# Kernel tuning notes

Measured on AMD Instinct MI355X. Metric: run time of the kernel, lower is better.

## Reference

```python
import jax, jax.numpy as jnp
import numpy as np

N, DZ, L, H, MLPH, INC = 256, 256, 256, 512, 2048, 8
CAT_IDX = np.arange(0, 192, 2)                      # 96 categorical token positions (interleaved)
NUM_IDX = np.setdiff1d(np.arange(L), CAT_IDX)       # 160 numerical token positions
CARDS = [4, 16, 128]                                # cardinality per categorical group
GSZ = 32                                            # tokens per categorical group
NUM_CARD = 100                                      # cardinality of quantized numerical params


def setup_inputs() -> dict:
    ks = list(jax.random.split(jax.random.key(0), 24))
    def nrm(shape, s=0.02):
        return jax.random.normal(ks.pop(), shape, jnp.float32) * s
    inp = {}
    inp['z'] = jax.random.normal(ks.pop(), (N, DZ), jnp.float32)
    inp['mlp_w0'] = nrm((DZ, MLPH)); inp['mlp_b0'] = jnp.zeros((MLPH,), jnp.float32)
    inp['mlp_w1'] = nrm((MLPH, MLPH)); inp['mlp_b1'] = jnp.zeros((MLPH,), jnp.float32)
    inp['mlp_w2'] = nrm((MLPH, MLPH)); inp['mlp_b2'] = jnp.zeros((MLPH,), jnp.float32)
    inp['conv_w'] = nrm((H, INC)); inp['conv_b'] = jnp.zeros((H,), jnp.float32)
    for g, card in enumerate(CARDS):
        inp[f'cat_w{g}'] = nrm((H, card)); inp[f'cat_b{g}'] = jnp.zeros((card,), jnp.float32)
    inp['num_w'] = nrm((H, 2)); inp['num_b'] = jnp.zeros((2,), jnp.float32)
    inp['num_target'] = jax.random.uniform(ks.pop(), (N, len(NUM_IDX)), jnp.float32)
    inp['cat_target'] = jax.random.randint(ks.pop(), (N, len(CAT_IDX)), 0, 4, jnp.int32)
    return inp


def reference(z, mlp_w0, mlp_b0, mlp_w1, mlp_b1, mlp_w2, mlp_b2, conv_w, conv_b,
              cat_w0, cat_b0, cat_w1, cat_b1, cat_w2, cat_b2, num_w, num_b,
              num_target, cat_target):
    n = z.shape[0]
    # MLP: fc0 -> act -> fc1 -> act -> fc2
    h = z @ mlp_w0 + mlp_b0
    h = jax.nn.relu(h) @ mlp_w1 + mlp_b1
    h = jax.nn.relu(h) @ mlp_w2 + mlp_b2
    h = h.reshape(n, INC, L)                        # (N, C=8, L)
    # act + 1x1 conv to hidden_size, then transpose -> (N, L, H)
    u = jnp.einsum('ncl,hc->nlh', jax.nn.relu(h), conv_w) + conv_b
    # ---- categorical tokens: gather, per-cardinality heads, CE NLL, argmax sample ----
    hc = u[:, CAT_IDX, :]                           # (N, 96, H)
    heads = [(cat_w0, cat_b0), (cat_w1, cat_b1), (cat_w2, cat_b2)]
    nlls, samps = [], []
    for g, (w, b) in enumerate(heads):
        hg = hc[:, g * GSZ:(g + 1) * GSZ, :]        # (N, 32, H)
        logits = hg @ w + b                         # (N, 32, card)
        logp = jax.nn.log_softmax(logits, axis=-1)
        tg = cat_target[:, g * GSZ:(g + 1) * GSZ]
        nlls.append(-jnp.take_along_axis(logp, tg[..., None], axis=-1)[..., 0])
        samps.append(jnp.argmax(logits, axis=-1))
    cat_nll = jnp.concatenate(nlls, axis=1)         # (N, 96)
    cat_samples = jnp.concatenate(samps, axis=1)    # (N, 96)
    # ---- numerical tokens: gather, 2-param discretized logistic, NLL, mode sample ----
    hn = u[:, NUM_IDX, :]                           # (N, 160, H)
    p = hn @ num_w + num_b                          # (N, 160, 2)
    mu = jax.nn.sigmoid(p[..., 0])
    s = jax.nn.softplus(p[..., 1]) + 1e-4
    hb = 1.0 / (2.0 * (NUM_CARD - 1))               # half bin width
    t = num_target
    cdf_p = jax.nn.sigmoid((t + hb - mu) / s)
    cdf_m = jax.nn.sigmoid((t - hb - mu) / s)
    prob = jnp.where(t < hb, cdf_p, jnp.where(t > 1.0 - hb, 1.0 - cdf_m, cdf_p - cdf_m))
    num_nll = -jnp.log(jnp.maximum(prob, 1e-7))     # (N, 160)
    num_samples = jax.lax.stop_gradient(jnp.round(mu * (NUM_CARD - 1)) / (NUM_CARD - 1))
    # ---- scatter samples back into the preallocated output tensor ----
    u_out = jnp.zeros((n, L, 3), jnp.float32)
    u_out = u_out.at[:, CAT_IDX, 0].set(cat_samples.astype(jnp.float32))
    u_out = u_out.at[:, NUM_IDX, 1].set(num_samples)
    return u_out, cat_nll, num_nll
```

## Files before the change

### kernel.cpp

```cpp
#include <hip/hip_runtime.h>
#include <hip/hip_fp16.h>
#include <math.h>

#define NN   256
#define LL   256
#define HH   512
#define MLPHv 2048
#define INCv 8
#define NCOLS 150

typedef _Float16 f16x8 __attribute__((ext_vector_type(8)));
typedef __fp16   fp16x2 __attribute__((ext_vector_type(2)));
typedef float    f32x4 __attribute__((ext_vector_type(4)));
typedef unsigned short ushort_t;

union u4f16 { uint4 u; f16x8 v; };
union u1f16 { fp16x2 h; unsigned u; };

__device__ __forceinline__ void split1(float f, ushort_t& h, ushort_t& l)
{
    __half hh = __float2half_rn(f);
    h = __half_as_ushort(hh);
    l = __half_as_ushort(__float2half_rn((f - __half2float(hh)) * 4096.f));
}

__device__ __forceinline__ void pack8(const float* fv, uint4& hv, uint4& lv)
{
    unsigned hw[4], lw[4];
#pragma unroll
    for (int p = 0; p < 4; ++p) {
        const float a = fv[2 * p], b = fv[2 * p + 1];
        u1f16 hc, lc;
        hc.h = __builtin_amdgcn_cvt_pkrtz(a, b);
        const float r0 = (a - (float)hc.h[0]) * 4096.f;
        const float r1 = (b - (float)hc.h[1]) * 4096.f;
        lc.h = __builtin_amdgcn_cvt_pkrtz(r0, r1);
        hw[p] = hc.u;
        lw[p] = lc.u;
    }
    hv.x = hw[0]; hv.y = hw[1]; hv.z = hw[2]; hv.w = hw[3];
    lv.x = lw[0]; lv.y = lw[1]; lv.z = lw[2]; lv.w = lw[3];
}

typedef __attribute__((address_space(3))) unsigned int lds_u32;
typedef __attribute__((address_space(1))) const unsigned int glb_u32;
__device__ __forceinline__ void gl_lds16(const ushort_t* g, ushort_t* l)
{
    __builtin_amdgcn_global_load_lds((glb_u32*)g, (lds_u32*)l, 16, 0, 0);
}
__device__ __forceinline__ void gl_lds16f(const float* g, float* l)
{
    __builtin_amdgcn_global_load_lds((glb_u32*)g, (lds_u32*)l, 16, 0, 0);
}


__global__ __launch_bounds__(256) void prep_small(
    const float* __restrict__ z,
    const float* __restrict__ cvw, const float* __restrict__ cvb,
    const float* __restrict__ cw0, const float* __restrict__ cb0,
    const float* __restrict__ cw1, const float* __restrict__ cb1,
    const float* __restrict__ cw2, const float* __restrict__ cb2,
    const float* __restrict__ nw,  const float* __restrict__ nbv,
    ushort_t* __restrict__ zh, ushort_t* __restrict__ zl,
    float* __restrict__ Mf, float* __restrict__ beta)
{
    const int bid = blockIdx.x;
    const int tid = threadIdx.x;
    if (bid < 16) {
        const int idx = bid * 256 + tid;
        const int r = idx >> 4, kq = idx & 15;
        const float* p = z + (size_t)r * 256 + kq * 16;
        float fv[16];
#pragma unroll
        for (int q = 0; q < 4; ++q) {
            float4 v = *(const float4*)(p + q * 4);
            fv[q * 4 + 0] = v.x; fv[q * 4 + 1] = v.y;
            fv[q * 4 + 2] = v.z; fv[q * 4 + 3] = v.w;
        }
        const int gm = r >> 4, l16 = r & 15;
#pragma unroll
        for (int o = 0; o < 2; ++o) {
            uint4 hv, lv;
            pack8(&fv[o * 8], hv, lv);
            const int koct = kq * 2 + o;
            const int ks = koct >> 2, koct3 = koct & 3;
            const size_t off = ((size_t)(gm * 8 + ks) * 64 + l16 + (koct3 << 4)) * 8;
            *(uint4*)&zh[off] = hv;
            *(uint4*)&zl[off] = lv;
        }
    } else {
        const int k = bid - 16;
        const float* W; const float* B; int off, card;
        if (k < 4)        { W = cw0; B = cb0; off = 0;   card = 4;   }
        else if (k < 20)  { W = cw1; B = cb1; off = 4;   card = 16;  }
        else if (k < 148) { W = cw2; B = cb2; off = 20;  card = 128; }
        else              { W = nw;  B = nbv; off = 148; card = 2;   }
        const int kc = k - off;
        float part[INCv + 1];
#pragma unroll
        for (int c = 0; c <= INCv; ++c) part[c] = 0.f;
#pragma unroll
        for (int it = 0; it < 2; ++it) {
            const int h = tid + it * 256;
            const float wv = W[h * card + kc];
#pragma unroll
            for (int c = 0; c < INCv; ++c) part[c] += cvw[h * INCv + c] * wv;
            part[INCv] += cvb[h] * wv;
        }
        __shared__ float red[INCv + 1][4];
        const int lane = tid & 63, wave = tid >> 6;
#pragma unroll
        for (int c = 0; c <= INCv; ++c) {
            float v = part[c];
#pragma unroll
            for (int o = 32; o >= 1; o >>= 1) v += __shfl_down(v, o, 64);
            if (lane == 0) red[c][wave] = v;
        }
        __syncthreads();
        if (tid <= INCv) {
            const float s = red[tid][0] + red[tid][1] + red[tid][2] + red[tid][3];
            if (tid < INCv) Mf[tid * NCOLS + k] = s;
            else            beta[k] = s + B[kc];
        }
    }
}

template <int OUT>
__global__ __launch_bounds__(512, 2) void gemm_v3(
    const ushort_t* __restrict__ Ah, const ushort_t* __restrict__ Al,
    const float* __restrict__ W, const float* __restrict__ bias,
    float* __restrict__ part, ushort_t* __restrict__ oH, ushort_t* __restrict__ oL,
    int KS32, int kchunk32, int steps)
{
    __shared__ ushort_t sAh[2][4096];
    __shared__ ushort_t sAl[2][4096];
    __shared__ float    sWf[2][4160];

    const int tid  = threadIdx.x;
    const int lane = tid & 63, w = tid >> 6;
    const int wr   = w >> 2, wc = w & 3;
    const int bx   = blockIdx.x, by = blockIdx.y, bz = blockIdx.z;
    const int bn   = bx * 64;
    const int kb0  = bz * kchunk32;

    f32x4 accH[2], accC[2];
#pragma unroll
    for (int r = 0; r < 2; ++r) {
        accH[r] = (f32x4){0.f, 0.f, 0.f, 0.f};
        accC[r] = (f32x4){0.f, 0.f, 0.f, 0.f};
    }

    auto STAGE = [&](int ts, int b) {
        const int kb = kb0 + ts * 2;
        const int g = w >> 1, ks = w & 1;
        const size_t fA = ((size_t)(by * 4 + g) * KS32 + kb + ks) * 512 + lane * 8;
        gl_lds16(Ah + fA, &sAh[b][w * 512]);
        gl_lds16(Al + fA, &sAl[b][w * 512]);
        const int k0 = kb * 32;
#pragma unroll
        for (int ii = 0; ii < 2; ++ii) {
            const int i = w * 2 + ii;
            const float* src = W + (size_t)(k0 + i * 4 + (lane >> 4)) * 2048 + bn + (lane & 15) * 4;
            gl_lds16f(src, &sWf[b][i * 260]);
        }
    };

    STAGE(0, 0);
    for (int t = 0; t < steps; ++t) {
        const int cur = t & 1;
        if (t + 1 < steps) {
            STAGE(t + 1, cur ^ 1);
            asm volatile("s_waitcnt vmcnt(4)" ::: "memory");
        } else {
            asm volatile("s_waitcnt vmcnt(0)" ::: "memory");
        }
        __builtin_amdgcn_s_barrier();
        asm volatile("" ::: "memory");

        f16x8 bH[2], bL[2];
#pragma unroll
        for (int ks = 0; ks < 2; ++ks) {
            const int col  = wc * 16 + (lane & 15);
            const int koct = lane >> 4;
            float fv[8];
#pragma unroll
            for (int j = 0; j < 8; ++j) {
                const int i = ks * 8 + koct * 2 + (j >> 2);
                fv[j] = sWf[cur][i * 260 + (j & 3) * 64 + col];
            }
            u4f16 hv, lv;
            pack8(fv, hv.u, lv.u);
            bH[ks] = hv.v;
            bL[ks] = lv.v;
        }

        __builtin_amdgcn_s_setprio(1);
#pragma unroll
        for (int ks = 0; ks < 2; ++ks) {
            f16x8 aH[2], aL[2];
#pragma unroll
            for (int r = 0; r < 2; ++r) {
                const int off = (((wr * 2 + r) * 2 + ks) * 64 + lane) * 8;
                aH[r] = *(const f16x8*)&sAh[cur][off];
                aL[r] = *(const f16x8*)&sAl[cur][off];
            }
#pragma unroll
            for (int r = 0; r < 2; ++r) {
                accH[r] = __builtin_amdgcn_mfma_f32_16x16x32_f16(aH[r], bH[ks], accH[r], 0, 0, 0);
                accC[r] = __builtin_amdgcn_mfma_f32_16x16x32_f16(aH[r], bL[ks], accC[r], 0, 0, 0);
                accC[r] = __builtin_amdgcn_mfma_f32_16x16x32_f16(aL[r], bH[ks], accC[r], 0, 0, 0);
            }
        }
        __builtin_amdgcn_s_setprio(0);
        __builtin_amdgcn_s_barrier();
        asm volatile("" ::: "memory");
    }

    const float inv = 1.f / 4096.f;
#pragma unroll
    for (int r = 0; r < 2; ++r) {
        const int row0 = by * 64 + (wr * 2 + r) * 16 + ((lane >> 4) << 2);
        const int col  = bn + wc * 16 + (lane & 15);
        if (OUT == 0) {
            float* po = part + (size_t)bz * 524288;
#pragma unroll
            for (int e = 0; e < 4; ++e)
                po[(size_t)(row0 + e) * 2048 + col] = accH[r][e] + accC[r][e] * inv;
        } else {
            const float vb = bias[col];
            const int gm = by * 4 + wr * 2 + r;
            const int ks = col >> 5, koct3 = (col >> 3) & 3, j = col & 7;
            const size_t fb = ((size_t)(gm * 64 + ks) * 64) * 8 + (koct3 << 4) * 8 + j;
#pragma unroll
            for (int e = 0; e < 4; ++e) {
                const float v = fmaxf(accH[r][e] + accC[r][e] * inv + vb, 0.f);
                ushort_t h, l;
                split1(v, h, l);
                const int l16 = ((lane >> 4) << 2) + e;
                oH[fb + (size_t)l16 * 8] = h;
                oL[fb + (size_t)l16 * 8] = l;
            }
        }
    }
}

__global__ __launch_bounds__(256) void reduce_pk(
    const float* __restrict__ part, const float* __restrict__ bias,
    ushort_t* __restrict__ oH, ushort_t* __restrict__ oL)
{
    const int b  = blockIdx.x;
    const int ct = b & 15, rg = b >> 4;
    const int e  = threadIdx.x * 4;
    const int row = rg * 8 + (e >> 7);
    const int col = ct * 128 + (e & 127);
    const size_t idx = (size_t)row * 2048 + col;
    float4 s = *(const float4*)&bias[col];
#pragma unroll
    for (int k = 0; k < 4; ++k) {
        const float4 p = *(const float4*)&part[(size_t)k * 524288 + idx];
        s.x += p.x; s.y += p.y; s.z += p.z; s.w += p.w;
    }
    s.x = fmaxf(s.x, 0.f); s.y = fmaxf(s.y, 0.f);
    s.z = fmaxf(s.z, 0.f); s.w = fmaxf(s.w, 0.f);
    ushort_t h[4], l[4];
    split1(s.x, h[0], l[0]); split1(s.y, h[1], l[1]);
    split1(s.z, h[2], l[2]); split1(s.w, h[3], l[3]);
    const int gm = row >> 4, l16 = row & 15;
    const int ks = col >> 5, koct3 = (col >> 3) & 3, j = col & 7;
    const size_t off = ((size_t)(gm * 64 + ks) * 64 + l16 + (koct3 << 4)) * 8 + j;
    ushort4 hv = {h[0], h[1], h[2], h[3]};
    ushort4 lv = {l[0], l[1], l[2], l[3]};
    *(ushort4*)&oH[off] = hv;
    *(ushort4*)&oL[off] = lv;
}

__global__ __launch_bounds__(256) void heads_kernel(
    const float* __restrict__ part, const float* __restrict__ b2,
    const float* __restrict__ Mf, const float* __restrict__ beta,
    const int* __restrict__ cat_target, const float* __restrict__ num_target,
    float* __restrict__ out)
{
    const int bx  = blockIdx.x;
    const int tid = threadIdx.x;
    __shared__ float Ms[INCv][128];
    __shared__ float Bsh[128];
    if (bx < 96) {
        const int g = bx >> 5;
        const int card = (g == 0) ? 4 : (g == 1) ? 16 : 128;
        const int off  = (g == 0) ? 0 : (g == 1) ? 4  : 20;
        for (int i = tid; i < card * INCv; i += 256) {
            int c = i / card, k = i % card;
            Ms[c][k] = Mf[c * NCOLS + off + k];
        }
        for (int i = tid; i < card; i += 256) Bsh[i] = beta[off + i];
        __syncthreads();

        const int idx = (bx & 31) * 256 + tid;
        const int n = idx >> 5, j = idx & 31;
        const int ci = g * 32 + j;
        const int l  = ci * 2;
        float rv[INCv];
#pragma unroll
        for (int c = 0; c < INCv; ++c) {
            const size_t e = (size_t)n * MLPHv + c * LL + l;
            float s = b2[c * LL + l];
#pragma unroll
            for (int k = 0; k < 4; ++k) s += part[(size_t)k * 524288 + e];
            rv[c] = fmaxf(s, 0.f);
        }

        float mx = -1e30f; int arg = 0;
        for (int k = 0; k < card; ++k) {
            float s = Bsh[k];
#pragma unroll
            for (int c = 0; c < INCv; ++c) s += rv[c] * Ms[c][k];
            if (s > mx) { mx = s; arg = k; }
        }
        const int tg = cat_target[n * 96 + ci];
        float sum = 0.f, stg = 0.f;
        for (int k = 0; k < card; ++k) {
            float s = Bsh[k];
#pragma unroll
            for (int c = 0; c < INCv; ++c) s += rv[c] * Ms[c][k];
            sum += expf(s - mx);
            if (k == tg) stg = s;
        }
        const float lse = mx + logf(sum);
        out[NN * LL * 3 + n * 96 + ci] = lse - stg;
        float* u = out + (size_t)(n * LL + l) * 3;
        u[0] = (float)arg; u[1] = 0.f; u[2] = 0.f;
    } else {
        const int idx = (bx - 96) * 256 + tid;
        const int n = idx / 160, ni = idx % 160;
        const int l = (ni < 96) ? (2 * ni + 1) : (96 + ni);
        float rv[INCv];
#pragma unroll
        for (int c = 0; c < INCv; ++c) {
            const size_t e = (size_t)n * MLPHv + c * LL + l;
            float s = b2[c * LL + l];
#pragma unroll
            for (int k = 0; k < 4; ++k) s += part[(size_t)k * 524288 + e];
            rv[c] = fmaxf(s, 0.f);
        }
        float p0 = beta[148], p1 = beta[149];
#pragma unroll
        for (int c = 0; c < INCv; ++c) {
            p0 += rv[c] * Mf[c * NCOLS + 148];
            p1 += rv[c] * Mf[c * NCOLS + 149];
        }
        const float mu = 1.f / (1.f + expf(-p0));
        const float sp = (p1 > 20.f) ? p1 : log1pf(expf(p1));
        const float s  = sp + 1e-4f;
        const float hb = 1.f / 198.f;
        const float t  = num_target[n * 160 + ni];
        const float cp = 1.f / (1.f + expf(-((t + hb - mu) / s)));
        const float cm = 1.f / (1.f + expf(-((t - hb - mu) / s)));
        const float prob = (t < hb) ? cp : ((t > 1.f - hb) ? (1.f - cm) : (cp - cm));
        out[NN * LL * 3 + NN * 96 + n * 160 + ni] = -logf(fmaxf(prob, 1e-7f));
        float* u = out + (size_t)(n * LL + l) * 3;
        u[0] = 0.f; u[1] = rintf(mu * 99.f) / 99.f; u[2] = 0.f;
    }
}

extern "C" void kernel_launch(void* const* d_in, const int* in_sizes, int n_in,
                              void* d_out, int out_size, void* d_ws, size_t ws_size,
                              hipStream_t stream)
{
    const float* z   = (const float*)d_in[0];
    const float* w0  = (const float*)d_in[1];
    const float* b0  = (const float*)d_in[2];
    const float* w1  = (const float*)d_in[3];
    const float* b1  = (const float*)d_in[4];
    const float* w2  = (const float*)d_in[5];
    const float* b2  = (const float*)d_in[6];
    const float* cvw = (const float*)d_in[7];
    const float* cvb = (const float*)d_in[8];
    const float* cw0 = (const float*)d_in[9];
    const float* cb0 = (const float*)d_in[10];
    const float* cw1 = (const float*)d_in[11];
    const float* cb1 = (const float*)d_in[12];
    const float* cw2 = (const float*)d_in[13];
    const float* cb2 = (const float*)d_in[14];
    const float* nw  = (const float*)d_in[15];
    const float* nb  = (const float*)d_in[16];
    const float* num_target = (const float*)d_in[17];
    const int*   cat_target = (const int*)d_in[18];
    float* out = (float*)d_out;
    float* ws  = (float*)d_ws;

    size_t o = 0;
    float*    part = ws + o;                o += 4ull * 524288;
    float*    Mf   = ws + o;                o += 1536;
    float*    beta = ws + o;                o += 256;
    ushort_t* zh   = (ushort_t*)(ws + o);   o += 32768;
    ushort_t* zl   = (ushort_t*)(ws + o);   o += 32768;
    ushort_t* r0h  = (ushort_t*)(ws + o);   o += 262144;
    ushort_t* r0l  = (ushort_t*)(ws + o);   o += 262144;
    ushort_t* r1h  = (ushort_t*)(ws + o);   o += 262144;
    ushort_t* r1l  = (ushort_t*)(ws + o);   o += 262144;

    prep_small<<<dim3(166), 256, 0, stream>>>(
        z, cvw, cvb, cw0, cb0, cw1, cb1, cw2, cb2, nw, nb, zh, zl, Mf, beta);

    gemm_v3<1><<<dim3(32, 4, 1), 512, 0, stream>>>(
        zh, zl, w0, b0, nullptr, r0h, r0l, 8, 8, 4);

    gemm_v3<0><<<dim3(32, 4, 4), 512, 0, stream>>>(
        r0h, r0l, w1, nullptr, part, nullptr, nullptr, 64, 16, 8);
    reduce_pk<<<dim3(512), 256, 0, stream>>>(part, b1, r1h, r1l);

    gemm_v3<0><<<dim3(32, 4, 4), 512, 0, stream>>>(
        r1h, r1l, w2, nullptr, part, nullptr, nullptr, 64, 16, 8);

    heads_kernel<<<dim3(256), 256, 0, stream>>>(
        part, b2, Mf, beta, cat_target, num_target, out);
}
```

Baseline: 67.94 us.

## Remove prep kernel: split z inside first GEMM, fold head weights in heads kernel

Drops the separate prep_small launch. The first GEMM gains an AMODE=1 path that loads fp32 z tiles directly into LDS and splits them into fp16 hi/lo on the fly. The folded conv×head weight matrices and biases are now computed inside each heads_kernel block. This removes one kernel launch and its global round trip. In exchange, every heads block redundantly runs 512-long serial dot products before its main work, which adds latency per block.

```diff
diff --git a/kernel.cpp b/kernel.cpp
--- a/kernel.cpp
+++ b/kernel.cpp
@@ -7,7 +7,6 @@
 #define HH   512
 #define MLPHv 2048
 #define INCv 8
-#define NCOLS 150
 
 typedef _Float16 f16x8 __attribute__((ext_vector_type(8)));
 typedef __fp16   fp16x2 __attribute__((ext_vector_type(2)));
@@ -54,87 +53,16 @@
 }
 
 
-__global__ __launch_bounds__(256) void prep_small(
-    const float* __restrict__ z,
-    const float* __restrict__ cvw, const float* __restrict__ cvb,
-    const float* __restrict__ cw0, const float* __restrict__ cb0,
-    const float* __restrict__ cw1, const float* __restrict__ cb1,
-    const float* __restrict__ cw2, const float* __restrict__ cb2,
-    const float* __restrict__ nw,  const float* __restrict__ nbv,
-    ushort_t* __restrict__ zh, ushort_t* __restrict__ zl,
-    float* __restrict__ Mf, float* __restrict__ beta)
-{
-    const int bid = blockIdx.x;
-    const int tid = threadIdx.x;
-    if (bid < 16) {
-        const int idx = bid * 256 + tid;
-        const int r = idx >> 4, kq = idx & 15;
-        const float* p = z + (size_t)r * 256 + kq * 16;
-        float fv[16];
-#pragma unroll
-        for (int q = 0; q < 4; ++q) {
-            float4 v = *(const float4*)(p + q * 4);
-            fv[q * 4 + 0] = v.x; fv[q * 4 + 1] = v.y;
-            fv[q * 4 + 2] = v.z; fv[q * 4 + 3] = v.w;
-        }
-        const int gm = r >> 4, l16 = r & 15;
-#pragma unroll
-        for (int o = 0; o < 2; ++o) {
-            uint4 hv, lv;
-            pack8(&fv[o * 8], hv, lv);
-            const int koct = kq * 2 + o;
-            const int ks = koct >> 2, koct3 = koct & 3;
-            const size_t off = ((size_t)(gm * 8 + ks) * 64 + l16 + (koct3 << 4)) * 8;
-            *(uint4*)&zh[off] = hv;
-            *(uint4*)&zl[off] = lv;
-        }
-    } else {
-        const int k = bid - 16;
-        const float* W; const float* B; int off, card;
-        if (k < 4)        { W = cw0; B = cb0; off = 0;   card = 4;   }
-        else if (k < 20)  { W = cw1; B = cb1; off = 4;   card = 16;  }
-        else if (k < 148) { W = cw2; B = cb2; off = 20;  card = 128; }
-        else              { W = nw;  B = nbv; off = 148; card = 2;   }
-        const int kc = k - off;
-        float part[INCv + 1];
-#pragma unroll
-        for (int c = 0; c <= INCv; ++c) part[c] = 0.f;
-#pragma unroll
-        for (int it = 0; it < 2; ++it) {
-            const int h = tid + it * 256;
-            const float wv = W[h * card + kc];
-#pragma unroll
-            for (int c = 0; c < INCv; ++c) part[c] += cvw[h * INCv + c] * wv;
-            part[INCv] += cvb[h] * wv;
-        }
-        __shared__ float red[INCv + 1][4];
-        const int lane = tid & 63, wave = tid >> 6;
-#pragma unroll
-        for (int c = 0; c <= INCv; ++c) {
-            float v = part[c];
-#pragma unroll
-            for (int o = 32; o >= 1; o >>= 1) v += __shfl_down(v, o, 64);
-            if (lane == 0) red[c][wave] = v;
-        }
-        __syncthreads();
-        if (tid <= INCv) {
-            const float s = red[tid][0] + red[tid][1] + red[tid][2] + red[tid][3];
-            if (tid < INCv) Mf[tid * NCOLS + k] = s;
-            else            beta[k] = s + B[kc];
-        }
-    }
-}
-
-template <int OUT>
+template <int OUT, int AMODE>
 __global__ __launch_bounds__(512, 2) void gemm_v3(
     const ushort_t* __restrict__ Ah, const ushort_t* __restrict__ Al,
+    const float* __restrict__ Af,
     const float* __restrict__ W, const float* __restrict__ bias,
     float* __restrict__ part, ushort_t* __restrict__ oH, ushort_t* __restrict__ oL,
-    int KS32, int kchunk32, int steps)
-{
-    __shared__ ushort_t sAh[2][4096];
-    __shared__ ushort_t sAl[2][4096];
-    __shared__ float    sWf[2][4160];
+    int KS32, int kchunk32, int steps, int K)
+{
+    __shared__ __align__(16) char sA_raw[2][16640];
+    __shared__ float sWf[2][4160];
 
     const int tid  = threadIdx.x;
     const int lane = tid & 63, w = tid >> 6;
@@ -152,10 +80,20 @@
 
     auto STAGE = [&](int ts, int b) {
         const int kb = kb0 + ts * 2;
-        const int g = w >> 1, ks = w & 1;
-        const size_t fA = ((size_t)(by * 4 + g) * KS32 + kb + ks) * 512 + lane * 8;
-        gl_lds16(Ah + fA, &sAh[b][w * 512]);
-        gl_lds16(Al + fA, &sAl[b][w * 512]);
+        if (AMODE == 0) {
+            const int g = w >> 1, ks = w & 1;
+            const size_t fA = ((size_t)(by * 4 + g) * KS32 + kb + ks) * 512 + lane * 8;
+            gl_lds16(Ah + fA, (ushort_t*)sA_raw[b] + w * 512);
+            gl_lds16(Al + fA, (ushort_t*)(sA_raw[b] + 8192) + w * 512);
+        } else {
+            const int k0 = kb * 32;
+#pragma unroll
+            for (int ii = 0; ii < 2; ++ii) {
+                const int i = w * 2 + ii;
+                const float* src = Af + (size_t)(by * 64 + i * 4 + (lane >> 4)) * K + k0 + (lane & 15) * 4;
+                gl_lds16f(src, (float*)sA_raw[b] + i * 260 + lane * 4);
+            }
+        }
         const int k0 = kb * 32;
 #pragma unroll
         for (int ii = 0; ii < 2; ++ii) {
@@ -200,9 +138,25 @@
             f16x8 aH[2], aL[2];
 #pragma unroll
             for (int r = 0; r < 2; ++r) {
-                const int off = (((wr * 2 + r) * 2 + ks) * 64 + lane) * 8;
-                aH[r] = *(const f16x8*)&sAh[cur][off];
-                aL[r] = *(const f16x8*)&sAl[cur][off];
+                if (AMODE == 0) {
+                    const int off = (((wr * 2 + r) * 2 + ks) * 64 + lane) * 8;
+                    aH[r] = *(const f16x8*)((const ushort_t*)sA_raw[cur] + off);
+                    aL[r] = *(const f16x8*)((const ushort_t*)(sA_raw[cur] + 8192) + off);
+                } else {
+                    const int row_l = wr * 32 + r * 16 + (lane & 15);
+                    const int base  = (row_l >> 2) * 260 + (row_l & 3) * 64
+                                    + ks * 32 + (lane >> 4) * 8;
+                    const float* p = (const float*)sA_raw[cur] + base;
+                    float fv[8];
+                    float4 v0 = *(const float4*)p;
+                    float4 v1 = *(const float4*)(p + 4);
+                    fv[0]=v0.x; fv[1]=v0.y; fv[2]=v0.z; fv[3]=v0.w;
+                    fv[4]=v1.x; fv[5]=v1.y; fv[6]=v1.z; fv[7]=v1.w;
+                    u4f16 hv, lv;
+                    pack8(fv, hv.u, lv.u);
+                    aH[r] = hv.v;
+                    aL[r] = lv.v;
+                }
             }
 #pragma unroll
             for (int r = 0; r < 2; ++r) {
@@ -276,23 +230,34 @@
 
 __global__ __launch_bounds__(256) void heads_kernel(
     const float* __restrict__ part, const float* __restrict__ b2,
-    const float* __restrict__ Mf, const float* __restrict__ beta,
+    const float* __restrict__ cvw, const float* __restrict__ cvb,
+    const float* __restrict__ cw0, const float* __restrict__ cb0,
+    const float* __restrict__ cw1, const float* __restrict__ cb1,
+    const float* __restrict__ cw2, const float* __restrict__ cb2,
+    const float* __restrict__ nw,  const float* __restrict__ nbv,
     const int* __restrict__ cat_target, const float* __restrict__ num_target,
     float* __restrict__ out)
 {
     const int bx  = blockIdx.x;
     const int tid = threadIdx.x;
-    __shared__ float Ms[INCv][128];
-    __shared__ float Bsh[128];
     if (bx < 96) {
+        __shared__ float Ms[INCv][128];
+        __shared__ float Bsh[128];
         const int g = bx >> 5;
         const int card = (g == 0) ? 4 : (g == 1) ? 16 : 128;
-        const int off  = (g == 0) ? 0 : (g == 1) ? 4  : 20;
-        for (int i = tid; i < card * INCv; i += 256) {
-            int c = i / card, k = i % card;
-            Ms[c][k] = Mf[c * NCOLS + off + k];
-        }
-        for (int i = tid; i < card; i += 256) Bsh[i] = beta[off + i];
+        const float* Wg = (g == 0) ? cw0 : (g == 1) ? cw1 : cw2;
+        const float* Bg = (g == 0) ? cb0 : (g == 1) ? cb1 : cb2;
+        for (int o = tid; o < card * 9; o += 256) {
+            const int kk = o / 9, c = o % 9;
+            float s = 0.f;
+            if (c < INCv) {
+                for (int h = 0; h < HH; ++h) s += cvw[h * INCv + c] * Wg[h * card + kk];
+                Ms[c][kk] = s;
+            } else {
+                for (int h = 0; h < HH; ++h) s += cvb[h] * Wg[h * card + kk];
+                Bsh[kk] = s + Bg[kk];
+            }
+        }
         __syncthreads();
 
         const int idx = (bx & 31) * 256 + tid;
@@ -330,6 +295,20 @@
         float* u = out + (size_t)(n * LL + l) * 3;
         u[0] = (float)arg; u[1] = 0.f; u[2] = 0.f;
     } else {
+        __shared__ float MB[18];
+        for (int o = tid; o < 18; o += 256) {
+            const int c = o >> 1, j = o & 1;
+            float s = 0.f;
+            if (c < INCv) {
+                for (int h = 0; h < HH; ++h) s += cvw[h * INCv + c] * nw[h * 2 + j];
+                MB[c * 2 + j] = s;
+            } else {
+                for (int h = 0; h < HH; ++h) s += cvb[h] * nw[h * 2 + j];
+                MB[16 + j] = s + nbv[j];
+            }
+        }
+        __syncthreads();
+
         const int idx = (bx - 96) * 256 + tid;
         const int n = idx / 160, ni = idx % 160;
         const int l = (ni < 96) ? (2 * ni + 1) : (96 + ni);
@@ -342,11 +321,11 @@
             for (int k = 0; k < 4; ++k) s += part[(size_t)k * 524288 + e];
             rv[c] = fmaxf(s, 0.f);
         }
-        float p0 = beta[148], p1 = beta[149];
+        float p0 = MB[16], p1 = MB[17];
 #pragma unroll
         for (int c = 0; c < INCv; ++c) {
-            p0 += rv[c] * Mf[c * NCOLS + 148];
-            p1 += rv[c] * Mf[c * NCOLS + 149];
+            p0 += rv[c] * MB[c * 2 + 0];
+            p1 += rv[c] * MB[c * 2 + 1];
         }
         const float mu = 1.f / (1.f + expf(-p0));
         const float sp = (p1 > 20.f) ? p1 : log1pf(expf(p1));
@@ -390,28 +369,22 @@
 
     size_t o = 0;
     float*    part = ws + o;                o += 4ull * 524288;
-    float*    Mf   = ws + o;                o += 1536;
-    float*    beta = ws + o;                o += 256;
-    ushort_t* zh   = (ushort_t*)(ws + o);   o += 32768;
-    ushort_t* zl   = (ushort_t*)(ws + o);   o += 32768;
     ushort_t* r0h  = (ushort_t*)(ws + o);   o += 262144;
     ushort_t* r0l  = (ushort_t*)(ws + o);   o += 262144;
     ushort_t* r1h  = (ushort_t*)(ws + o);   o += 262144;
     ushort_t* r1l  = (ushort_t*)(ws + o);   o += 262144;
 
-    prep_small<<<dim3(166), 256, 0, stream>>>(
-        z, cvw, cvb, cw0, cb0, cw1, cb1, cw2, cb2, nw, nb, zh, zl, Mf, beta);
-
-    gemm_v3<1><<<dim3(32, 4, 1), 512, 0, stream>>>(
-        zh, zl, w0, b0, nullptr, r0h, r0l, 8, 8, 4);
-
-    gemm_v3<0><<<dim3(32, 4, 4), 512, 0, stream>>>(
-        r0h, r0l, w1, nullptr, part, nullptr, nullptr, 64, 16, 8);
+    gemm_v3<1, 1><<<dim3(32, 4, 1), 512, 0, stream>>>(
+        nullptr, nullptr, z, w0, b0, nullptr, r0h, r0l, 8, 8, 4, 256);
+
+    gemm_v3<0, 0><<<dim3(32, 4, 4), 512, 0, stream>>>(
+        r0h, r0l, nullptr, w1, nullptr, part, nullptr, nullptr, 64, 16, 8, 2048);
     reduce_pk<<<dim3(512), 256, 0, stream>>>(part, b1, r1h, r1l);
 
-    gemm_v3<0><<<dim3(32, 4, 4), 512, 0, stream>>>(
-        r1h, r1l, w2, nullptr, part, nullptr, nullptr, 64, 16, 8);
+    gemm_v3<0, 0><<<dim3(32, 4, 4), 512, 0, stream>>>(
+        r1h, r1l, nullptr, w2, nullptr, part, nullptr, nullptr, 64, 16, 8, 2048);
 
     heads_kernel<<<dim3(256), 256, 0, stream>>>(
-        part, b2, Mf, beta, cat_target, num_target, out);
-}
+        part, b2, cvw, cvb, cw0, cb0, cw1, cb1, cw2, cb2, nw, nb,
+        cat_target, num_target, out);
+}
```

Measured after the change: 232.7 us. +242.5%, slower.
